# Performance work log

Hardware: AMD Instinct MI355X
Metric: run time of the kernel (lower is better)

The kernel has to match this reference:

```python
import jax, jax.numpy as jnp
import numpy as np

N, C, HW = 32, 256, 64          # batch, in_channels, input_size
K = 128                          # n_clusters
S = 8                            # blocks per side
BLOCK = (HW + S - 1) // S        # = 8, padding_size = 0


def setup_inputs() -> dict:
    key = jax.random.key(0)
    k1, k2 = jax.random.split(key)
    x = jax.random.normal(k1, (N, C, HW, HW), dtype=jnp.float32)
    cluster_centers = jax.random.normal(k2, (K, C), dtype=jnp.float32)
    return {"x": x, "cluster_centers": cluster_centers}


def reference(x, cluster_centers):
    # --- Codebook: argmin over squared distances, computed without the
    x2 = jnp.sum(x * x, axis=1)                       # (N, H, W)
    c2 = jnp.sum(cluster_centers * cluster_centers, axis=1)  # (K,)
    xc = jnp.einsum('nchw,kc->nkhw', x, cluster_centers)     # (N, K, H, W)
    dist = x2[:, None] - 2.0 * xc + c2[None, :, None, None]
    code = jnp.argmin(dist, axis=1)                   # (N, H, W) int

    # --- BlockWiseHistogramEncoder: unfold into S*S non-overlapping
    # BLOCKxBLOCK blocks (padding_size == 0 here), one_hot(code+1), mean ---
    shifted = code + 1                                # values in [1, K]
    n = shifted.shape[0]
    blocks = shifted.reshape(n, S, BLOCK, S, BLOCK)
    blocks = blocks.transpose(0, 1, 3, 2, 4).reshape(n, S * S, BLOCK * BLOCK)
    onehot = (blocks[..., None] == jnp.arange(K + 1)).astype(jnp.float32)
    return onehot.mean(axis=2)                        # (N, S*S, K+1)
```

## Files before the change

### kernel.cpp

```cpp
#include <hip/hip_runtime.h>

#define C_DIM 256
#define K_DIM 128
#define HW_DIM 64
#define PIX 4096
#define N_IMG 32

using short8 = __attribute__((ext_vector_type(8))) short;
using f32x4  = __attribute__((ext_vector_type(4))) float;

__device__ __forceinline__ void lds_barrier() {
    asm volatile("s_waitcnt lgkmcnt(0)\n\ts_barrier" ::: "memory");
}

__device__ __forceinline__ unsigned long long umin64(unsigned long long a, unsigned long long b) {
    return a < b ? a : b;
}
__device__ __forceinline__ unsigned mono(float d) {
    unsigned u = __float_as_uint(d);
    return u ^ ((u & 0x80000000u) ? 0xFFFFFFFFu : 0x80000000u);
}

__device__ __forceinline__ void split3t(float v, unsigned& hu, unsigned& mu, unsigned& lu) {
    unsigned u = __float_as_uint(v);
    unsigned hf = u & 0xffff0000u;
    float r1 = v - __uint_as_float(hf);
    unsigned r1u = __float_as_uint(r1);
    unsigned mf = r1u & 0xffff0000u;
    float r2 = r1 - __uint_as_float(mf);
    hu = u; mu = r1u; lu = __float_as_uint(r2);
}

__global__ __launch_bounds__(64) void prep_kernel(const float* __restrict__ cl,
                                                  unsigned short* __restrict__ Bt,
                                                  float* __restrict__ c2) {
    int k = blockIdx.x;
    int lane = threadIdx.x;
    const float4* row = (const float4*)(cl + k * C_DIM);
    float4 v = row[lane];
    float vv[4] = {v.x, v.y, v.z, v.w};
    unsigned short* bk = Bt + k * 768 + lane * 4;
#pragma unroll
    for (int i = 0; i < 4; ++i) {
        unsigned hu, mu, lu;
        split3t(vv[i], hu, mu, lu);
        bk[i]       = (unsigned short)(hu >> 16);
        bk[256 + i] = (unsigned short)(mu >> 16);
        bk[512 + i] = (unsigned short)(lu >> 16);
    }
    if (lane == 0) {
        float s = 0.f;
#pragma unroll
        for (int i = 0; i < C_DIM / 4; ++i) {
            float4 u = row[i];
            s = fmaf(u.x, u.x, s);
            s = fmaf(u.y, u.y, s);
            s = fmaf(u.z, u.z, s);
            s = fmaf(u.w, u.w, s);
        }
        c2[k] = s;
    }
}

__global__ __launch_bounds__(256) void main_kernel(
    const float* __restrict__ x, const unsigned short* __restrict__ Bt,
    const float* __restrict__ c2v, unsigned char* __restrict__ code) {

    __shared__ __align__(16) unsigned short Ap[3 * 4096];
    __shared__ float x2p[2][128];
    unsigned long long* red = (unsigned long long*)Ap;

    const int t    = threadIdx.x;
    const int lane = t & 63;
    const int w    = t >> 6;
    const int q    = lane >> 4;
    const int l15  = lane & 15;

    const int px = t & 127;
    const int h  = t >> 7;

    const int b   = blockIdx.x;
    const int img = b >> 5;
    const int pb  = (b & 31) * 128;

    const float* xg = x + (size_t)img * (C_DIM * PIX) + pb + px;

    f32x4 acc[8][2];
#pragma unroll
    for (int m = 0; m < 8; ++m)
#pragma unroll
        for (int ns = 0; ns < 2; ++ns) acc[m][ns] = (f32x4){0.f, 0.f, 0.f, 0.f};

    float xr[16];
#pragma unroll
    for (int j = 0; j < 16; ++j) xr[j] = xg[(size_t)(h * 16 + j) * PIX];

    float x2part = 0.f;
    const unsigned short* btb = Bt + (w * 32 + l15) * 768 + q * 8;

    const int wbase = (px >> 4) * 512 + (px & 15) * 8 + h * 2 * 128;

#pragma unroll 1
    for (int ci = 0; ci < 8; ++ci) {
        short8 bv[3][2];
#pragma unroll
        for (int p = 0; p < 3; ++p) {
            bv[p][0] = *(const short8*)(btb + p * 256 + ci * 32);
            bv[p][1] = *(const short8*)(btb + 16 * 768 + p * 256 + ci * 32);
        }

#pragma unroll
        for (int g = 0; g < 2; ++g) {
            unsigned p0[4], p1[4], p2[4];
#pragma unroll
            for (int jj = 0; jj < 4; ++jj) {
                float v0 = xr[g * 8 + jj * 2], v1 = xr[g * 8 + jj * 2 + 1];
                unsigned h0, m0, l0, h1, m1, l1;
                split3t(v0, h0, m0, l0);
                split3t(v1, h1, m1, l1);
                p0[jj] = (h0 >> 16) | (h1 & 0xffff0000u);
                p1[jj] = (m0 >> 16) | (m1 & 0xffff0000u);
                p2[jj] = (l0 >> 16) | (l1 & 0xffff0000u);
                x2part = fmaf(v0, v0, x2part);
                x2part = fmaf(v1, v1, x2part);
            }
            int base = wbase + g * 128;
            *(uint4*)&Ap[base]            = make_uint4(p0[0], p0[1], p0[2], p0[3]);
            *(uint4*)&Ap[4096 + base]     = make_uint4(p1[0], p1[1], p1[2], p1[3]);
            *(uint4*)&Ap[8192 + base]     = make_uint4(p2[0], p2[1], p2[2], p2[3]);
        }
        if (ci == 7) x2p[h][px] = x2part;

        if (ci < 7) {
#pragma unroll
            for (int j = 0; j < 16; ++j)
                xr[j] = xg[(size_t)((ci + 1) * 32 + h * 16 + j) * PIX];
        }

        lds_barrier();

#pragma unroll
        for (int pa = 0; pa < 3; ++pa) {
#pragma unroll
            for (int mg = 0; mg < 4; ++mg) {
                const int m0 = mg * 2, m1 = mg * 2 + 1;
                short8 af0 = *(const short8*)&Ap[pa * 4096 + m0 * 512 + lane * 8];
                short8 af1 = *(const short8*)&Ap[pa * 4096 + m1 * 512 + lane * 8];
#pragma unroll
                for (int pb2 = 0; pb2 < 3; ++pb2) {
                    if (pb2 < 3 - pa) {
                        acc[m0][0] = __builtin_amdgcn_mfma_f32_16x16x32_bf16(af0, bv[pb2][0], acc[m0][0], 0, 0, 0);
                        acc[m0][1] = __builtin_amdgcn_mfma_f32_16x16x32_bf16(af0, bv[pb2][1], acc[m0][1], 0, 0, 0);
                        acc[m1][0] = __builtin_amdgcn_mfma_f32_16x16x32_bf16(af1, bv[pb2][0], acc[m1][0], 0, 0, 0);
                        acc[m1][1] = __builtin_amdgcn_mfma_f32_16x16x32_bf16(af1, bv[pb2][1], acc[m1][1], 0, 0, 0);
                    }
                }
            }
        }
        lds_barrier();
    }

    const float c2a0 = c2v[w * 32 + l15];
    const float c2a1 = c2v[w * 32 + 16 + l15];
    const unsigned n0 = (unsigned)(w * 32 + l15);
    const unsigned n1 = n0 + 16;

#pragma unroll
    for (int m = 0; m < 8; ++m) {
#pragma unroll
        for (int r = 0; r < 4; ++r) {
            int pxl = m * 16 + q * 4 + r;
            float x2v = x2p[0][pxl] + x2p[1][pxl];
            float d0 = (x2v - 2.0f * acc[m][0][r]) + c2a0;
            float d1 = (x2v - 2.0f * acc[m][1][r]) + c2a1;
            unsigned long long k0 = ((unsigned long long)mono(d0) << 32) | n0;
            unsigned long long k1 = ((unsigned long long)mono(d1) << 32) | n1;
            unsigned long long best = umin64(k0, k1);
            best = umin64(best, __shfl_xor(best, 1));
            best = umin64(best, __shfl_xor(best, 2));
            best = umin64(best, __shfl_xor(best, 4));
            best = umin64(best, __shfl_xor(best, 8));
            if (l15 == 0) red[w * 128 + pxl] = best;
        }
    }
    lds_barrier();

    if (t < 128) {
        unsigned long long m0 = umin64(umin64(red[t], red[128 + t]),
                                       umin64(red[256 + t], red[384 + t]));
        code[(size_t)img * PIX + pb + t] = (unsigned char)(m0 & 0xFFu);
    }
}

__global__ __launch_bounds__(256) void hist_kernel(const unsigned char* __restrict__ code,
                                                   float* __restrict__ out) {
    __shared__ int hist[4][K_DIM + 1];
    int wid = threadIdx.x >> 6, lane = threadIdx.x & 63;
    int b = blockIdx.x * 4 + wid;
    int n = b >> 6, sy = (b >> 3) & 7, sx = b & 7;

    hist[wid][lane] = 0;
    hist[wid][lane + 64] = 0;
    if (lane == 0) hist[wid][128] = 0;
    __syncthreads();

    int hh = sy * 8 + (lane >> 3);
    int ww = sx * 8 + (lane & 7);
    int c = code[n * PIX + hh * HW_DIM + ww];
    atomicAdd(&hist[wid][c + 1], 1);
    __syncthreads();

    const float inv = 1.0f / 64.0f;
    out[(size_t)b * (K_DIM + 1) + lane] = hist[wid][lane] * inv;
    out[(size_t)b * (K_DIM + 1) + 64 + lane] = hist[wid][lane + 64] * inv;
    if (lane == 0) out[(size_t)b * (K_DIM + 1) + 128] = hist[wid][128] * inv;
}

extern "C" void kernel_launch(void* const* d_in, const int* in_sizes, int n_in,
                              void* d_out, int out_size, void* d_ws, size_t ws_size,
                              hipStream_t stream) {
    const float* x  = (const float*)d_in[0];
    const float* cl = (const float*)d_in[1];
    float* out = (float*)d_out;

    unsigned short* Bt = (unsigned short*)d_ws;
    float* c2 = (float*)((char*)d_ws + 196608);
    unsigned char* code = (unsigned char*)d_ws + 197120;

    prep_kernel<<<K_DIM, 64, 0, stream>>>(cl, Bt, c2);
    main_kernel<<<(N_IMG * PIX) / 128, 256, 0, stream>>>(x, Bt, c2, code);
    hist_kernel<<<(N_IMG * 64) / 4, 256, 0, stream>>>(code, out);
}
```

Before: 227.1 us.

## Double-buffer the LDS A tile so conversion overlaps MFMA work

After: 224.1 us. No clear change (-1.3%).

```diff
diff --git a/kernel.cpp b/kernel.cpp
--- a/kernel.cpp
+++ b/kernel.cpp
@@ -62,11 +62,55 @@
     }
 }
 
+__device__ __forceinline__ void convert_tile(const float xr[16], unsigned short* Aw,
+                                             int wbase, float& x2part) {
+#pragma unroll
+    for (int g = 0; g < 2; ++g) {
+        unsigned p0[4], p1[4], p2[4];
+#pragma unroll
+        for (int jj = 0; jj < 4; ++jj) {
+            float v0 = xr[g * 8 + jj * 2], v1 = xr[g * 8 + jj * 2 + 1];
+            unsigned h0, m0, l0, h1, m1, l1;
+            split3t(v0, h0, m0, l0);
+            split3t(v1, h1, m1, l1);
+            p0[jj] = (h0 >> 16) | (h1 & 0xffff0000u);
+            p1[jj] = (m0 >> 16) | (m1 & 0xffff0000u);
+            p2[jj] = (l0 >> 16) | (l1 & 0xffff0000u);
+            x2part = fmaf(v0, v0, x2part);
+            x2part = fmaf(v1, v1, x2part);
+        }
+        int base = wbase + g * 128;
+        *(uint4*)&Aw[base]        = make_uint4(p0[0], p0[1], p0[2], p0[3]);
+        *(uint4*)&Aw[4096 + base] = make_uint4(p1[0], p1[1], p1[2], p1[3]);
+        *(uint4*)&Aw[8192 + base] = make_uint4(p2[0], p2[1], p2[2], p2[3]);
+    }
+}
+
+__device__ __forceinline__ void mfma_block(const unsigned short* Ac, const short8 bv[3][2],
+                                           f32x4 acc[8][2], int lane) {
+#pragma unroll
+    for (int pa = 0; pa < 3; ++pa) {
+#pragma unroll
+        for (int mg = 0; mg < 4; ++mg) {
+            const int m0 = mg * 2, m1 = mg * 2 + 1;
+            short8 af0 = *(const short8*)&Ac[pa * 4096 + m0 * 512 + lane * 8];
+            short8 af1 = *(const short8*)&Ac[pa * 4096 + m1 * 512 + lane * 8];
+#pragma unroll
+            for (int pb2 = 0; pb2 < 3 - pa; ++pb2) {
+                acc[m0][0] = __builtin_amdgcn_mfma_f32_16x16x32_bf16(af0, bv[pb2][0], acc[m0][0], 0, 0, 0);
+                acc[m0][1] = __builtin_amdgcn_mfma_f32_16x16x32_bf16(af0, bv[pb2][1], acc[m0][1], 0, 0, 0);
+                acc[m1][0] = __builtin_amdgcn_mfma_f32_16x16x32_bf16(af1, bv[pb2][0], acc[m1][0], 0, 0, 0);
+                acc[m1][1] = __builtin_amdgcn_mfma_f32_16x16x32_bf16(af1, bv[pb2][1], acc[m1][1], 0, 0, 0);
+            }
+        }
+    }
+}
+
 __global__ __launch_bounds__(256) void main_kernel(
     const float* __restrict__ x, const unsigned short* __restrict__ Bt,
     const float* __restrict__ c2v, unsigned char* __restrict__ code) {
 
-    __shared__ __align__(16) unsigned short Ap[3 * 4096];
+    __shared__ __align__(16) unsigned short Ap[2][12288];
     __shared__ float x2p[2][128];
     unsigned long long* red = (unsigned long long*)Ap;
 
@@ -83,7 +127,7 @@
     const int img = b >> 5;
     const int pb  = (b & 31) * 128;
 
-    const float* xg = x + (size_t)img * (C_DIM * PIX) + pb + px;
+    const float* xb = x + (size_t)img * (C_DIM * PIX) + pb;
 
     f32x4 acc[8][2];
 #pragma unroll
@@ -93,15 +137,20 @@
 
     float xr[16];
 #pragma unroll
-    for (int j = 0; j < 16; ++j) xr[j] = xg[(size_t)(h * 16 + j) * PIX];
+    for (int j = 0; j < 16; ++j) xr[j] = xb[(h * 16 + j) * PIX + px];
 
     float x2part = 0.f;
     const unsigned short* btb = Bt + (w * 32 + l15) * 768 + q * 8;
 
     const int wbase = (px >> 4) * 512 + (px & 15) * 8 + h * 2 * 128;
 
+    convert_tile(xr, Ap[0], wbase, x2part);
+#pragma unroll
+    for (int j = 0; j < 16; ++j) xr[j] = xb[(32 + h * 16 + j) * PIX + px];
+    lds_barrier();
+
 #pragma unroll 1
-    for (int ci = 0; ci < 8; ++ci) {
+    for (int ci = 0; ci < 7; ++ci) {
         short8 bv[3][2];
 #pragma unroll
         for (int p = 0; p < 3; ++p) {
@@ -109,54 +158,27 @@
             bv[p][1] = *(const short8*)(btb + 16 * 768 + p * 256 + ci * 32);
         }
 
-#pragma unroll
-        for (int g = 0; g < 2; ++g) {
-            unsigned p0[4], p1[4], p2[4];
-#pragma unroll
-            for (int jj = 0; jj < 4; ++jj) {
-                float v0 = xr[g * 8 + jj * 2], v1 = xr[g * 8 + jj * 2 + 1];
-                unsigned h0, m0, l0, h1, m1, l1;
-                split3t(v0, h0, m0, l0);
-                split3t(v1, h1, m1, l1);
-                p0[jj] = (h0 >> 16) | (h1 & 0xffff0000u);
-                p1[jj] = (m0 >> 16) | (m1 & 0xffff0000u);
-                p2[jj] = (l0 >> 16) | (l1 & 0xffff0000u);
-                x2part = fmaf(v0, v0, x2part);
-                x2part = fmaf(v1, v1, x2part);
-            }
-            int base = wbase + g * 128;
-            *(uint4*)&Ap[base]            = make_uint4(p0[0], p0[1], p0[2], p0[3]);
-            *(uint4*)&Ap[4096 + base]     = make_uint4(p1[0], p1[1], p1[2], p1[3]);
-            *(uint4*)&Ap[8192 + base]     = make_uint4(p2[0], p2[1], p2[2], p2[3]);
-        }
-        if (ci == 7) x2p[h][px] = x2part;
-
-        if (ci < 7) {
-#pragma unroll
-            for (int j = 0; j < 16; ++j)
-                xr[j] = xg[(size_t)((ci + 1) * 32 + h * 16 + j) * PIX];
-        }
+        convert_tile(xr, Ap[(ci + 1) & 1], wbase, x2part);
+        x2p[h][px] = x2part;
+
+        const int tnext = (ci + 2) & 7;
+#pragma unroll
+        for (int j = 0; j < 16; ++j)
+            xr[j] = xb[(tnext * 32 + h * 16 + j) * PIX + px];
+
+        mfma_block(Ap[ci & 1], bv, acc, lane);
 
         lds_barrier();
-
-#pragma unroll
-        for (int pa = 0; pa < 3; ++pa) {
-#pragma unroll
-            for (int mg = 0; mg < 4; ++mg) {
-                const int m0 = mg * 2, m1 = mg * 2 + 1;
-                short8 af0 = *(const short8*)&Ap[pa * 4096 + m0 * 512 + lane * 8];
-                short8 af1 = *(const short8*)&Ap[pa * 4096 + m1 * 512 + lane * 8];
-#pragma unroll
-                for (int pb2 = 0; pb2 < 3; ++pb2) {
-                    if (pb2 < 3 - pa) {
-                        acc[m0][0] = __builtin_amdgcn_mfma_f32_16x16x32_bf16(af0, bv[pb2][0], acc[m0][0], 0, 0, 0);
-                        acc[m0][1] = __builtin_amdgcn_mfma_f32_16x16x32_bf16(af0, bv[pb2][1], acc[m0][1], 0, 0, 0);
-                        acc[m1][0] = __builtin_amdgcn_mfma_f32_16x16x32_bf16(af1, bv[pb2][0], acc[m1][0], 0, 0, 0);
-                        acc[m1][1] = __builtin_amdgcn_mfma_f32_16x16x32_bf16(af1, bv[pb2][1], acc[m1][1], 0, 0, 0);
-                    }
-                }
-            }
-        }
+    }
+
+    {
+        short8 bv[3][2];
+#pragma unroll
+        for (int p = 0; p < 3; ++p) {
+            bv[p][0] = *(const short8*)(btb + p * 256 + 7 * 32);
+            bv[p][1] = *(const short8*)(btb + 16 * 768 + p * 256 + 7 * 32);
+        }
+        mfma_block(Ap[1], bv, acc, lane);
         lds_barrier();
     }
 
```
